# Kernel optimization log

Measured on AMD Instinct MI355X. Metric: run time of the kernel, lower is better.

## Reference

```python
import jax, jax.numpy as jnp
import numpy as np

# pywt db4 decomposition filters (8 taps)
DEC_LO = np.array([-0.010597401784997278, 0.032883011666982945, 0.030841381835986965,
                   -0.18703481171888114, -0.02798376941698385, 0.6308807679295904,
                   0.7148465705525415, 0.23037781330885523], dtype=np.float32)
DEC_HI = np.array([-0.23037781330885523, 0.7148465705525415, -0.6308807679295904,
                   -0.02798376941698385, 0.18703481171888114, 0.030841381835986965,
                   -0.032883011666982945, -0.010597401784997278], dtype=np.float32)
LEVEL = 6
F = 8  # filter length

# pywt dwt with mode='zero' is exactly full_convolve(x, filt)[1::2].
# We realize it as a strided correlation with the flipped filters:
# out[i] = sum_j x_pad[2i+j] * filt[F-1-j], x padded left by F-2 zeros.
_KERNEL = jnp.asarray(np.stack([DEC_LO[::-1], DEC_HI[::-1]])[:, None, :])  # [2,1,F]

def _dwt_step(x):
    # x: [B, N] -> (cA [B, M], cD [B, M]) with M = floor((N+F-1)/2)
    N = x.shape[-1]
    M = (N + F - 1) // 2
    xp = jnp.pad(x, ((0, 0), (F - 2, F)))[:, None, :]          # [B,1,Npad]
    y = jax.lax.conv_general_dilated(
        xp, _KERNEL.astype(x.dtype), window_strides=(2,), padding='VALID',
        dimension_numbers=('NCH', 'OIH', 'NCH'))                # [B,2,>=M]
    return y[:, 0, :M], y[:, 1, :M]


def setup_inputs() -> dict:
    key = jax.random.key(0)
    x = jax.random.normal(key, (64, 262144), dtype=jnp.float32)
    return {"x": x}


def reference(x):
    # Cascaded 6-level db4 DWT, zero boundary mode.
    a = x
    details = []  # finest first
    for _ in range(LEVEL):
        a, d = _dwt_step(a)
        details.append(d)
    # Match torch module: details[0] = coarsest detail (pywt coeffs[1])
    return (a,) + tuple(details[::-1])
```

## Files before the change

kernel.cpp:

```cpp
#include <hip/hip_runtime.h>


#define NT 256
#define TT 32
#define LEN0 2426
#define LEN1 1210
#define LEN2 602
#define LEN3 298
#define LEN4 146
#define LEN5 70

#define N0 262144
#define M1 131075
#define M2 65541
#define M3 32774
#define M4 16390
#define M5 8198
#define M6 4102

#define OFF_A6 ((size_t)0)
#define OFF_D6 ((size_t)262528)
#define OFF_D5 ((size_t)525056)
#define OFF_D4 ((size_t)1049728)
#define OFF_D3 ((size_t)2098688)
#define OFF_D2 ((size_t)4196224)
#define OFF_D1 ((size_t)8390848)

#define AE 0
#define AO 1216
#define BE 2432
#define BO 3040
#define LDS_FLOATS 3648

__device__ __constant__ float RLO[8] = {
    0.23037781330885523f, 0.7148465705525415f, 0.6308807679295904f,
    -0.02798376941698385f, -0.18703481171888114f, 0.030841381835986965f,
    0.032883011666982945f, -0.010597401784997278f};
__device__ __constant__ float RHI[8] = {
    -0.010597401784997278f, -0.032883011666982945f, 0.030841381835986965f,
    0.18703481171888114f, -0.02798376941698385f, -0.6308807679295904f,
    0.7148465705525415f, -0.23037781330885523f};

template <int LEN, int NC, int SHIFT>
__device__ __forceinline__ void level_fast(const float4* __restrict__ sE4,
                                           const float4* __restrict__ sO4,
                                           float2* __restrict__ dE2,
                                           float2* __restrict__ dO2,
                                           float* __restrict__ dg) {
  for (int c = threadIdx.x; c < NC; c += NT) {
    float4 e0 = sE4[c], e1 = sE4[c + 1];
    float4 o0 = sO4[c], o1 = sO4[c + 1];
    float e[8] = {e0.x, e0.y, e0.z, e0.w, e1.x, e1.y, e1.z, e1.w};
    float o[8] = {o0.x, o0.y, o0.z, o0.w, o1.x, o1.y, o1.z, o1.w};
    float a[4], d[4];
#pragma unroll
    for (int j = 0; j < 4; ++j) {
      float aa = 0.f, dd = 0.f;
#pragma unroll
      for (int t = 0; t < 4; ++t) {
        float ev = e[j + t + SHIFT];
        float ov = o[j + t + SHIFT];
        aa = fmaf(RLO[2 * t], ev, aa);
        aa = fmaf(RLO[2 * t + 1], ov, aa);
        dd = fmaf(RHI[2 * t], ev, dd);
        dd = fmaf(RHI[2 * t + 1], ov, dd);
      }
      a[j] = aa;
      d[j] = dd;
    }
    dE2[c] = make_float2(a[0], a[2]);
    dO2[c] = make_float2(a[1], a[3]);
    const int l0 = 4 * c;
    if (l0 + 4 <= LEN) {
#pragma unroll
      for (int j = 0; j < 4; ++j) __builtin_nontemporal_store(d[j], dg + l0 + j);
    } else {
#pragma unroll
      for (int j = 0; j < 4; ++j)
        if (l0 + j < LEN) __builtin_nontemporal_store(d[j], dg + l0 + j);
    }
  }
}

__device__ inline void dwt_step_slow(const float* __restrict__ s,
                                     float* __restrict__ d, int base, int len,
                                     int M, int cOff, float* __restrict__ dglob,
                                     int tid) {
  for (int l = tid; l < len; l += NT) {
    int g = base + l;
    float a = 0.f, dt = 0.f;
    if (g >= 0 && g < M) {
#pragma unroll
      for (int m = 0; m < 8; ++m) {
        float v = s[2 * l + m];
        a = fmaf(RLO[m], v, a);
        dt = fmaf(RHI[m], v, dt);
      }
    }
    d[l] = a;
    if (l >= cOff && g < M) dglob[g] = dt;
  }
}

__global__ __launch_bounds__(NT, 8) void dwt6_kernel(const float* __restrict__ x,
                                                     float* __restrict__ out) {
  const int p = blockIdx.x;
  const int row = blockIdx.y;
  const int tid = threadIdx.x;

  __shared__ float lds[LDS_FLOATS];

  const int b6 = p * TT;
  const int b5 = 2 * b6 - 6;
  const int b4 = 2 * b5 - 6;
  const int b3 = 2 * b4 - 6;
  const int b2 = 2 * b3 - 6;
  const int b1 = 2 * b2 - 6;
  const int b0 = 2 * b1 - 6;

  const size_t r1 = (size_t)row * M1, r2 = (size_t)row * M2,
               r3 = (size_t)row * M3, r4 = (size_t)row * M4,
               r5 = (size_t)row * M5, r6 = (size_t)row * M6;

  if (p >= 1 && p <= 127) {
    const float4* __restrict__ xs4 =
        (const float4*)(x + (size_t)row * N0 + (b0 - 2));
    float2* __restrict__ aE2 = (float2*)(lds + AE);
    float2* __restrict__ aO2 = (float2*)(lds + AO);
    for (int m = tid; m < 607; m += NT) {
      float4 v = xs4[m];
      aE2[m] = make_float2(v.x, v.z);
      aO2[m] = make_float2(v.y, v.w);
    }
    __syncthreads();

    const float4* aE4 = (const float4*)(lds + AE);
    const float4* aO4 = (const float4*)(lds + AO);
    const float4* bE4 = (const float4*)(lds + BE);
    const float4* bO4 = (const float4*)(lds + BO);
    float2* bE2 = (float2*)(lds + BE);
    float2* bO2 = (float2*)(lds + BO);

    level_fast<LEN1, 303, 1>(aE4, aO4, bE2, bO2, out + OFF_D1 + r1 + b1);
    __syncthreads();
    level_fast<LEN2, 151, 0>(bE4, bO4, aE2, aO2, out + OFF_D2 + r2 + b2);
    __syncthreads();
    level_fast<LEN3, 75, 0>(aE4, aO4, bE2, bO2, out + OFF_D3 + r3 + b3);
    __syncthreads();
    level_fast<LEN4, 37, 0>(bE4, bO4, aE2, aO2, out + OFF_D4 + r4 + b4);
    __syncthreads();
    level_fast<LEN5, 18, 0>(aE4, aO4, bE2, bO2, out + OFF_D5 + r5 + b5);
    __syncthreads();

    float* __restrict__ ga = out + OFF_A6 + r6 + b6;
    float* __restrict__ gd = out + OFF_D6 + r6 + b6;
    for (int c = tid; c < 8; c += NT) {
      float4 e0 = bE4[c], e1 = bE4[c + 1];
      float4 o0 = bO4[c], o1 = bO4[c + 1];
      float e[8] = {e0.x, e0.y, e0.z, e0.w, e1.x, e1.y, e1.z, e1.w};
      float o[8] = {o0.x, o0.y, o0.z, o0.w, o1.x, o1.y, o1.z, o1.w};
#pragma unroll
      for (int j = 0; j < 4; ++j) {
        float aa = 0.f, dd = 0.f;
#pragma unroll
        for (int t = 0; t < 4; ++t) {
          aa = fmaf(RLO[2 * t], e[j + t], aa);
          aa = fmaf(RLO[2 * t + 1], o[j + t], aa);
          dd = fmaf(RHI[2 * t], e[j + t], dd);
          dd = fmaf(RHI[2 * t + 1], o[j + t], dd);
        }
        __builtin_nontemporal_store(aa, ga + 4 * c + j);
        __builtin_nontemporal_store(dd, gd + 4 * c + j);
      }
    }
  } else {
    float* bufA = lds;
    float* bufB = lds + BE;
    const float* __restrict__ xr = x + (size_t)row * N0;
    for (int l = tid; l < LEN0; l += NT) {
      int g = b0 + l;
      bufA[l] = (g >= 0 && g < N0) ? xr[g] : 0.0f;
    }
    __syncthreads();

    dwt_step_slow(bufA, bufB, b1, LEN1, M1, 186, out + OFF_D1 + r1, tid);
    __syncthreads();
    dwt_step_slow(bufB, bufA, b2, LEN2, M2, 90, out + OFF_D2 + r2, tid);
    __syncthreads();
    dwt_step_slow(bufA, bufB, b3, LEN3, M3, 42, out + OFF_D3 + r3, tid);
    __syncthreads();
    dwt_step_slow(bufB, bufA, b4, LEN4, M4, 18, out + OFF_D4 + r4, tid);
    __syncthreads();
    dwt_step_slow(bufA, bufB, b5, LEN5, M5, 6, out + OFF_D5 + r5, tid);
    __syncthreads();

    for (int l = tid; l < TT; l += NT) {
      int g = b6 + l;
      if (g < M6) {
        float a = 0.f, dt = 0.f;
#pragma unroll
        for (int m = 0; m < 8; ++m) {
          float v = bufB[2 * l + m];
          a = fmaf(RLO[m], v, a);
          dt = fmaf(RHI[m], v, dt);
        }
        out[OFF_A6 + r6 + g] = a;
        out[OFF_D6 + r6 + g] = dt;
      }
    }
  }
}

extern "C" void kernel_launch(void* const* d_in, const int* in_sizes, int n_in,
                              void* d_out, int out_size, void* d_ws,
                              size_t ws_size, hipStream_t stream) {
  const float* x = (const float*)d_in[0];
  float* out = (float*)d_out;
  dim3 grid(129, 64);
  dwt6_kernel<<<grid, NT, 0, stream>>>(x, out);
}
```

Before: 115.8 us.

## Make blocks persistent over four tiles with register-prefetched next input

Each block now processes four consecutive tiles per row instead of one, with a separate block handling both edge tiles. While level 1 of the current tile runs, the next tile's input is loaded into registers, and it is written into the freed staging LDS after level 1 finishes. Barriers are replaced by an lgkmcnt wait plus s_barrier. This cuts the grid to a quarter of its size and overlaps global load latency with compute. In exchange there are fewer blocks to hide latency, more LDS per block, and extra register pressure from the prefetched values.

```diff
diff --git a/kernel.cpp b/kernel.cpp
--- a/kernel.cpp
+++ b/kernel.cpp
@@ -3,12 +3,7 @@
 
 #define NT 256
 #define TT 32
-#define LEN0 2426
-#define LEN1 1210
-#define LEN2 602
-#define LEN3 298
-#define LEN4 146
-#define LEN5 70
+#define ITERS 4
 
 #define N0 262144
 #define M1 131075
@@ -18,6 +13,18 @@
 #define M5 8198
 #define M6 4102
 
+#define LEN1 1210
+#define LEN2 602
+#define LEN3 298
+#define LEN4 146
+#define LEN5 70
+
+#define NC1 303
+#define NC2 151
+#define NC3 75
+#define NC4 37
+#define NC5 18
+
 #define OFF_A6 ((size_t)0)
 #define OFF_D6 ((size_t)262528)
 #define OFF_D5 ((size_t)525056)
@@ -26,11 +33,13 @@
 #define OFF_D2 ((size_t)4196224)
 #define OFF_D1 ((size_t)8390848)
 
-#define AE 0
-#define AO 1216
-#define BE 2432
-#define BO 3040
-#define LDS_FLOATS 3648
+#define SE 0
+#define SO 1216
+#define W0E 2432
+#define W0O 3040
+#define W1E 3648
+#define W1O 3952
+#define LDS_FLOATS 4256
 
 __device__ __constant__ float RLO[8] = {
     0.23037781330885523f, 0.7148465705525415f, 0.6308807679295904f,
@@ -40,6 +49,11 @@
     -0.010597401784997278f, -0.032883011666982945f, 0.030841381835986965f,
     0.18703481171888114f, -0.02798376941698385f, -0.6308807679295904f,
     0.7148465705525415f, -0.23037781330885523f};
+
+__device__ __forceinline__ void bar_lds() {
+  asm volatile("s_waitcnt lgkmcnt(0)" ::: "memory");
+  __builtin_amdgcn_s_barrier();
+}
 
 template <int LEN, int NC, int SHIFT>
 __device__ __forceinline__ void level_fast(const float4* __restrict__ sE4,
@@ -102,110 +116,173 @@
   }
 }
 
-__global__ __launch_bounds__(NT, 8) void dwt6_kernel(const float* __restrict__ x,
-                                                     float* __restrict__ out) {
-  const int p = blockIdx.x;
+__global__ __launch_bounds__(NT, 8) void dwt6_kernel(
+    const float* __restrict__ x, float* __restrict__ out) {
+  const int px = blockIdx.x;
   const int row = blockIdx.y;
   const int tid = threadIdx.x;
 
-  __shared__ float lds[LDS_FLOATS];
-
-  const int b6 = p * TT;
-  const int b5 = 2 * b6 - 6;
-  const int b4 = 2 * b5 - 6;
-  const int b3 = 2 * b4 - 6;
-  const int b2 = 2 * b3 - 6;
-  const int b1 = 2 * b2 - 6;
-  const int b0 = 2 * b1 - 6;
-
+  __shared__ __align__(16) float lds[LDS_FLOATS];
+
+  const float* __restrict__ xr = x + (size_t)row * N0;
   const size_t r1 = (size_t)row * M1, r2 = (size_t)row * M2,
                r3 = (size_t)row * M3, r4 = (size_t)row * M4,
                r5 = (size_t)row * M5, r6 = (size_t)row * M6;
 
-  if (p >= 1 && p <= 127) {
-    const float4* __restrict__ xs4 =
-        (const float4*)(x + (size_t)row * N0 + (b0 - 2));
-    float2* __restrict__ aE2 = (float2*)(lds + AE);
-    float2* __restrict__ aO2 = (float2*)(lds + AO);
-    for (int m = tid; m < 607; m += NT) {
-      float4 v = xs4[m];
-      aE2[m] = make_float2(v.x, v.z);
-      aO2[m] = make_float2(v.y, v.w);
-    }
-    __syncthreads();
-
-    const float4* aE4 = (const float4*)(lds + AE);
-    const float4* aO4 = (const float4*)(lds + AO);
-    const float4* bE4 = (const float4*)(lds + BE);
-    const float4* bO4 = (const float4*)(lds + BO);
-    float2* bE2 = (float2*)(lds + BE);
-    float2* bO2 = (float2*)(lds + BO);
-
-    level_fast<LEN1, 303, 1>(aE4, aO4, bE2, bO2, out + OFF_D1 + r1 + b1);
-    __syncthreads();
-    level_fast<LEN2, 151, 0>(bE4, bO4, aE2, aO2, out + OFF_D2 + r2 + b2);
-    __syncthreads();
-    level_fast<LEN3, 75, 0>(aE4, aO4, bE2, bO2, out + OFF_D3 + r3 + b3);
-    __syncthreads();
-    level_fast<LEN4, 37, 0>(bE4, bO4, aE2, aO2, out + OFF_D4 + r4 + b4);
-    __syncthreads();
-    level_fast<LEN5, 18, 0>(aE4, aO4, bE2, bO2, out + OFF_D5 + r5 + b5);
-    __syncthreads();
-
-    float* __restrict__ ga = out + OFF_A6 + r6 + b6;
-    float* __restrict__ gd = out + OFF_D6 + r6 + b6;
-    for (int c = tid; c < 8; c += NT) {
-      float4 e0 = bE4[c], e1 = bE4[c + 1];
-      float4 o0 = bO4[c], o1 = bO4[c + 1];
-      float e[8] = {e0.x, e0.y, e0.z, e0.w, e1.x, e1.y, e1.z, e1.w};
-      float o[8] = {o0.x, o0.y, o0.z, o0.w, o1.x, o1.y, o1.z, o1.w};
-#pragma unroll
-      for (int j = 0; j < 4; ++j) {
-        float aa = 0.f, dd = 0.f;
-#pragma unroll
-        for (int t = 0; t < 4; ++t) {
-          aa = fmaf(RLO[2 * t], e[j + t], aa);
-          aa = fmaf(RLO[2 * t + 1], o[j + t], aa);
-          dd = fmaf(RHI[2 * t], e[j + t], dd);
-          dd = fmaf(RHI[2 * t + 1], o[j + t], dd);
-        }
-        __builtin_nontemporal_store(aa, ga + 4 * c + j);
-        __builtin_nontemporal_store(dd, gd + 4 * c + j);
+  if (px < 32) {
+    float2* sE2 = (float2*)(lds + SE);
+    float2* sO2 = (float2*)(lds + SO);
+    const float4* sE4 = (const float4*)(lds + SE);
+    const float4* sO4 = (const float4*)(lds + SO);
+    float2* w0E2 = (float2*)(lds + W0E);
+    float2* w0O2 = (float2*)(lds + W0O);
+    float2* w1E2 = (float2*)(lds + W1E);
+    float2* w1O2 = (float2*)(lds + W1O);
+    const float4* w0E4 = (const float4*)(lds + W0E);
+    const float4* w0O4 = (const float4*)(lds + W0O);
+    const float4* w1E4 = (const float4*)(lds + W1E);
+    const float4* w1O4 = (const float4*)(lds + W1O);
+
+    const int p0 = 1 + ITERS * px;
+
+    {
+      const float4* __restrict__ xs4 = (const float4*)(xr + (2048 * p0 - 380));
+      float4 v0 = xs4[tid];
+      float4 v1, v2;
+      if (tid < 351) v1 = xs4[tid + 256];
+      if (tid < 95) v2 = xs4[tid + 512];
+      sE2[tid] = make_float2(v0.x, v0.z);
+      sO2[tid] = make_float2(v0.y, v0.w);
+      if (tid < 351) {
+        sE2[tid + 256] = make_float2(v1.x, v1.z);
+        sO2[tid + 256] = make_float2(v1.y, v1.w);
+      }
+      if (tid < 95) {
+        sE2[tid + 512] = make_float2(v2.x, v2.z);
+        sO2[tid + 512] = make_float2(v2.y, v2.w);
+      }
+    }
+
+#pragma unroll 1
+    for (int k = 0; k < ITERS; ++k) {
+      const int p = p0 + k;
+      if (p > 127) break;
+      const bool have_next = (k + 1 < ITERS) && (p + 1 <= 127);
+
+      float4 q0, q1, q2;
+      if (have_next) {
+        const float4* __restrict__ xn4 =
+            (const float4*)(xr + (2048 * (p + 1) - 380));
+        q0 = xn4[tid];
+        if (tid < 351) q1 = xn4[tid + 256];
+        if (tid < 95) q2 = xn4[tid + 512];
+      }
+
+      const int b6 = p * TT;
+      const int b5 = 2 * b6 - 6;
+      const int b4 = 2 * b5 - 6;
+      const int b3 = 2 * b4 - 6;
+      const int b2 = 2 * b3 - 6;
+      const int b1 = 2 * b2 - 6;
+
+      bar_lds();
+
+      level_fast<LEN1, NC1, 1>(sE4, sO4, w0E2, w0O2, out + OFF_D1 + r1 + b1);
+      bar_lds();
+
+      if (have_next) {
+        sE2[tid] = make_float2(q0.x, q0.z);
+        sO2[tid] = make_float2(q0.y, q0.w);
+        if (tid < 351) {
+          sE2[tid + 256] = make_float2(q1.x, q1.z);
+          sO2[tid + 256] = make_float2(q1.y, q1.w);
+        }
+        if (tid < 95) {
+          sE2[tid + 512] = make_float2(q2.x, q2.z);
+          sO2[tid + 512] = make_float2(q2.y, q2.w);
+        }
+      }
+
+      level_fast<LEN2, NC2, 0>(w0E4, w0O4, w1E2, w1O2,
+                               out + OFF_D2 + r2 + b2);
+      bar_lds();
+      level_fast<LEN3, NC3, 0>(w1E4, w1O4, w0E2, w0O2,
+                               out + OFF_D3 + r3 + b3);
+      bar_lds();
+      level_fast<LEN4, NC4, 0>(w0E4, w0O4, w1E2, w1O2,
+                               out + OFF_D4 + r4 + b4);
+      bar_lds();
+      level_fast<LEN5, NC5, 0>(w1E4, w1O4, w0E2, w0O2,
+                               out + OFF_D5 + r5 + b5);
+      bar_lds();
+
+      float* __restrict__ ga = out + OFF_A6 + r6 + b6;
+      float* __restrict__ gd = out + OFF_D6 + r6 + b6;
+      for (int c = tid; c < 8; c += NT) {
+        float4 e0 = w0E4[c], e1 = w0E4[c + 1];
+        float4 o0 = w0O4[c], o1 = w0O4[c + 1];
+        float e[8] = {e0.x, e0.y, e0.z, e0.w, e1.x, e1.y, e1.z, e1.w};
+        float o[8] = {o0.x, o0.y, o0.z, o0.w, o1.x, o1.y, o1.z, o1.w};
+#pragma unroll
+        for (int j = 0; j < 4; ++j) {
+          float aa = 0.f, dd = 0.f;
+#pragma unroll
+          for (int t = 0; t < 4; ++t) {
+            aa = fmaf(RLO[2 * t], e[j + t], aa);
+            aa = fmaf(RLO[2 * t + 1], o[j + t], aa);
+            dd = fmaf(RHI[2 * t], e[j + t], dd);
+            dd = fmaf(RHI[2 * t + 1], o[j + t], dd);
+          }
+          __builtin_nontemporal_store(aa, ga + 4 * c + j);
+          __builtin_nontemporal_store(dd, gd + 4 * c + j);
+        }
       }
     }
   } else {
-    float* bufA = lds;
-    float* bufB = lds + BE;
-    const float* __restrict__ xr = x + (size_t)row * N0;
-    for (int l = tid; l < LEN0; l += NT) {
-      int g = b0 + l;
-      bufA[l] = (g >= 0 && g < N0) ? xr[g] : 0.0f;
-    }
-    __syncthreads();
-
-    dwt_step_slow(bufA, bufB, b1, LEN1, M1, 186, out + OFF_D1 + r1, tid);
-    __syncthreads();
-    dwt_step_slow(bufB, bufA, b2, LEN2, M2, 90, out + OFF_D2 + r2, tid);
-    __syncthreads();
-    dwt_step_slow(bufA, bufB, b3, LEN3, M3, 42, out + OFF_D3 + r3, tid);
-    __syncthreads();
-    dwt_step_slow(bufB, bufA, b4, LEN4, M4, 18, out + OFF_D4 + r4, tid);
-    __syncthreads();
-    dwt_step_slow(bufA, bufB, b5, LEN5, M5, 6, out + OFF_D5 + r5, tid);
-    __syncthreads();
-
-    for (int l = tid; l < TT; l += NT) {
-      int g = b6 + l;
-      if (g < M6) {
-        float a = 0.f, dt = 0.f;
-#pragma unroll
-        for (int m = 0; m < 8; ++m) {
-          float v = bufB[2 * l + m];
-          a = fmaf(RLO[m], v, a);
-          dt = fmaf(RHI[m], v, dt);
-        }
-        out[OFF_A6 + r6 + g] = a;
-        out[OFF_D6 + r6 + g] = dt;
+    float* A = lds;
+    float* B = lds + W0E;
+#pragma unroll 1
+    for (int t = 0; t < 2; ++t) {
+      const int p = (t == 0) ? 0 : 128;
+      const int b6 = p * TT;
+      const int b5 = 2 * b6 - 6;
+      const int b4 = 2 * b5 - 6;
+      const int b3 = 2 * b4 - 6;
+      const int b2 = 2 * b3 - 6;
+      const int b1 = 2 * b2 - 6;
+      const int b0 = 2 * b1 - 6;
+
+      bar_lds();
+      for (int l = tid; l < 2426; l += NT) {
+        int g = b0 + l;
+        A[l] = (g >= 0 && g < N0) ? xr[g] : 0.0f;
+      }
+      bar_lds();
+
+      dwt_step_slow(A, B, b1, LEN1, M1, 186, out + OFF_D1 + r1, tid);
+      bar_lds();
+      dwt_step_slow(B, A, b2, LEN2, M2, 90, out + OFF_D2 + r2, tid);
+      bar_lds();
+      dwt_step_slow(A, B, b3, LEN3, M3, 42, out + OFF_D3 + r3, tid);
+      bar_lds();
+      dwt_step_slow(B, A, b4, LEN4, M4, 18, out + OFF_D4 + r4, tid);
+      bar_lds();
+      dwt_step_slow(A, B, b5, LEN5, M5, 6, out + OFF_D5 + r5, tid);
+      bar_lds();
+
+      for (int l = tid; l < TT; l += NT) {
+        int g = b6 + l;
+        if (g < M6) {
+          float a = 0.f, dt = 0.f;
+#pragma unroll
+          for (int m = 0; m < 8; ++m) {
+            float v = B[2 * l + m];
+            a = fmaf(RLO[m], v, a);
+            dt = fmaf(RHI[m], v, dt);
+          }
+          out[OFF_A6 + r6 + g] = a;
+          out[OFF_D6 + r6 + g] = dt;
+        }
       }
     }
   }
@@ -216,6 +293,6 @@
                               size_t ws_size, hipStream_t stream) {
   const float* x = (const float*)d_in[0];
   float* out = (float*)d_out;
-  dim3 grid(129, 64);
+  dim3 grid(33, 64);
   dwt6_kernel<<<grid, NT, 0, stream>>>(x, out);
 }
```

After: 124.6 us. 7.6% more time.

## Give each wavefront its own DWT tile and drop block-wide barriers

Applied to the files above, without the earlier changes.

Tiles are halved and each of the four wavefronts in a block now runs its own independent 6-level cascade in a private LDS slice. Block-wide __syncthreads are replaced by a wave-local lgkmcnt wait. The first level is computed directly from global float4 loads, removing the LDS staging pass. The boundary tiles (p=0, 255, 256) are handled in a loop by one extra block per row, and the grid shrinks accordingly. The cost is more halo recomputation per output from the smaller tiles, and correctness depends on the wave-local LDS fence being enough for intra-wave LDS reuse.

```diff
diff --git a/kernel.cpp b/kernel.cpp
--- a/kernel.cpp
+++ b/kernel.cpp
@@ -2,13 +2,7 @@
 
 
 #define NT 256
-#define TT 32
-#define LEN0 2426
-#define LEN1 1210
-#define LEN2 602
-#define LEN3 298
-#define LEN4 146
-#define LEN5 70
+#define TT 16
 
 #define N0 262144
 #define M1 131075
@@ -18,6 +12,19 @@
 #define M5 8198
 #define M6 4102
 
+#define NC1 190
+#define NC2 94
+#define NC3 46
+#define NC4 22
+#define NC5 10
+
+#define LEN0S 1402
+#define LEN1S 698
+#define LEN2S 346
+#define LEN3S 170
+#define LEN4S 82
+#define LEN5S 38
+
 #define OFF_A6 ((size_t)0)
 #define OFF_D6 ((size_t)262528)
 #define OFF_D5 ((size_t)525056)
@@ -26,11 +33,12 @@
 #define OFF_D2 ((size_t)4196224)
 #define OFF_D1 ((size_t)8390848)
 
-#define AE 0
-#define AO 1216
-#define BE 2432
-#define BO 3040
-#define LDS_FLOATS 3648
+#define W0E 0
+#define W0O 384
+#define W1E 768
+#define W1O 960
+#define WSLICE 1152
+#define LDS_FLOATS (4 * WSLICE)
 
 __device__ __constant__ float RLO[8] = {
     0.23037781330885523f, 0.7148465705525415f, 0.6308807679295904f,
@@ -41,44 +49,48 @@
     0.18703481171888114f, -0.02798376941698385f, -0.6308807679295904f,
     0.7148465705525415f, -0.23037781330885523f};
 
-template <int LEN, int NC, int SHIFT>
-__device__ __forceinline__ void level_fast(const float4* __restrict__ sE4,
-                                           const float4* __restrict__ sO4,
-                                           float2* __restrict__ dE2,
-                                           float2* __restrict__ dO2,
-                                           float* __restrict__ dg) {
-  for (int c = threadIdx.x; c < NC; c += NT) {
+__device__ __forceinline__ void fence_lds() {
+  asm volatile("s_waitcnt lgkmcnt(0)" ::: "memory");
+}
+
+template <int SHIFT>
+__device__ __forceinline__ void conv8(const float e[8], const float o[8],
+                                      float a[4], float d[4]) {
+#pragma unroll
+  for (int j = 0; j < 4; ++j) {
+    float aa = 0.f, dd = 0.f;
+#pragma unroll
+    for (int t = 0; t < 4; ++t) {
+      float ev = e[j + t + SHIFT];
+      float ov = o[j + t + SHIFT];
+      aa = fmaf(RLO[2 * t], ev, aa);
+      aa = fmaf(RLO[2 * t + 1], ov, aa);
+      dd = fmaf(RHI[2 * t], ev, dd);
+      dd = fmaf(RHI[2 * t + 1], ov, dd);
+    }
+    a[j] = aa;
+    d[j] = dd;
+  }
+}
+
+template <int NC>
+__device__ __forceinline__ void level_w(const float4* __restrict__ sE4,
+                                        const float4* __restrict__ sO4,
+                                        float2* __restrict__ dE2,
+                                        float2* __restrict__ dO2,
+                                        float* __restrict__ dg, int lane) {
+  for (int c = lane; c < NC; c += 64) {
     float4 e0 = sE4[c], e1 = sE4[c + 1];
     float4 o0 = sO4[c], o1 = sO4[c + 1];
     float e[8] = {e0.x, e0.y, e0.z, e0.w, e1.x, e1.y, e1.z, e1.w};
     float o[8] = {o0.x, o0.y, o0.z, o0.w, o1.x, o1.y, o1.z, o1.w};
     float a[4], d[4];
-#pragma unroll
-    for (int j = 0; j < 4; ++j) {
-      float aa = 0.f, dd = 0.f;
-#pragma unroll
-      for (int t = 0; t < 4; ++t) {
-        float ev = e[j + t + SHIFT];
-        float ov = o[j + t + SHIFT];
-        aa = fmaf(RLO[2 * t], ev, aa);
-        aa = fmaf(RLO[2 * t + 1], ov, aa);
-        dd = fmaf(RHI[2 * t], ev, dd);
-        dd = fmaf(RHI[2 * t + 1], ov, dd);
-      }
-      a[j] = aa;
-      d[j] = dd;
-    }
+    conv8<0>(e, o, a, d);
     dE2[c] = make_float2(a[0], a[2]);
     dO2[c] = make_float2(a[1], a[3]);
     const int l0 = 4 * c;
-    if (l0 + 4 <= LEN) {
-#pragma unroll
-      for (int j = 0; j < 4; ++j) __builtin_nontemporal_store(d[j], dg + l0 + j);
-    } else {
-#pragma unroll
-      for (int j = 0; j < 4; ++j)
-        if (l0 + j < LEN) __builtin_nontemporal_store(d[j], dg + l0 + j);
-    }
+#pragma unroll
+    for (int j = 0; j < 4; ++j) __builtin_nontemporal_store(d[j], dg + l0 + j);
   }
 }
 
@@ -102,110 +114,138 @@
   }
 }
 
-__global__ __launch_bounds__(NT, 8) void dwt6_kernel(const float* __restrict__ x,
-                                                     float* __restrict__ out) {
-  const int p = blockIdx.x;
+__global__ __launch_bounds__(NT, 8) void dwt6_kernel(
+    const float* __restrict__ x, float* __restrict__ out) {
+  const int px = blockIdx.x;
   const int row = blockIdx.y;
   const int tid = threadIdx.x;
 
-  __shared__ float lds[LDS_FLOATS];
-
-  const int b6 = p * TT;
-  const int b5 = 2 * b6 - 6;
-  const int b4 = 2 * b5 - 6;
-  const int b3 = 2 * b4 - 6;
-  const int b2 = 2 * b3 - 6;
-  const int b1 = 2 * b2 - 6;
-  const int b0 = 2 * b1 - 6;
-
+  __shared__ __align__(16) float lds[LDS_FLOATS];
+
+  const float* __restrict__ xr = x + (size_t)row * N0;
   const size_t r1 = (size_t)row * M1, r2 = (size_t)row * M2,
                r3 = (size_t)row * M3, r4 = (size_t)row * M4,
                r5 = (size_t)row * M5, r6 = (size_t)row * M6;
 
-  if (p >= 1 && p <= 127) {
-    const float4* __restrict__ xs4 =
-        (const float4*)(x + (size_t)row * N0 + (b0 - 2));
-    float2* __restrict__ aE2 = (float2*)(lds + AE);
-    float2* __restrict__ aO2 = (float2*)(lds + AO);
-    for (int m = tid; m < 607; m += NT) {
-      float4 v = xs4[m];
-      aE2[m] = make_float2(v.x, v.z);
-      aO2[m] = make_float2(v.y, v.w);
-    }
-    __syncthreads();
-
-    const float4* aE4 = (const float4*)(lds + AE);
-    const float4* aO4 = (const float4*)(lds + AO);
-    const float4* bE4 = (const float4*)(lds + BE);
-    const float4* bO4 = (const float4*)(lds + BO);
-    float2* bE2 = (float2*)(lds + BE);
-    float2* bO2 = (float2*)(lds + BO);
-
-    level_fast<LEN1, 303, 1>(aE4, aO4, bE2, bO2, out + OFF_D1 + r1 + b1);
-    __syncthreads();
-    level_fast<LEN2, 151, 0>(bE4, bO4, aE2, aO2, out + OFF_D2 + r2 + b2);
-    __syncthreads();
-    level_fast<LEN3, 75, 0>(aE4, aO4, bE2, bO2, out + OFF_D3 + r3 + b3);
-    __syncthreads();
-    level_fast<LEN4, 37, 0>(bE4, bO4, aE2, aO2, out + OFF_D4 + r4 + b4);
-    __syncthreads();
-    level_fast<LEN5, 18, 0>(aE4, aO4, bE2, bO2, out + OFF_D5 + r5 + b5);
-    __syncthreads();
-
-    float* __restrict__ ga = out + OFF_A6 + r6 + b6;
-    float* __restrict__ gd = out + OFF_D6 + r6 + b6;
-    for (int c = tid; c < 8; c += NT) {
-      float4 e0 = bE4[c], e1 = bE4[c + 1];
-      float4 o0 = bO4[c], o1 = bO4[c + 1];
+  if (px < 64) {
+    const int wv = tid >> 6;
+    const int lane = tid & 63;
+    const int p = 1 + 4 * px + wv;
+    if (p > 254) return;
+
+    float* __restrict__ W = lds + wv * WSLICE;
+    float2* w0E2 = (float2*)(W + W0E);
+    float2* w0O2 = (float2*)(W + W0O);
+    float2* w1E2 = (float2*)(W + W1E);
+    float2* w1O2 = (float2*)(W + W1O);
+    const float4* w0E4 = (const float4*)(W + W0E);
+    const float4* w0O4 = (const float4*)(W + W0O);
+    const float4* w1E4 = (const float4*)(W + W1E);
+    const float4* w1O4 = (const float4*)(W + W1O);
+
+    const int b6 = 16 * p;
+    const int b5 = 32 * p - 6;
+    const int b4 = 64 * p - 18;
+    const int b3 = 128 * p - 42;
+    const int b2 = 256 * p - 90;
+    const int b1 = 512 * p - 186;
+
+    {
+      const float4* __restrict__ x4 = (const float4*)(xr + (1024 * p - 380));
+      float* __restrict__ dg1 = out + OFF_D1 + r1 + b1;
+      for (int c = lane; c < NC1; c += 64) {
+        float4 q0 = x4[2 * c], q1 = x4[2 * c + 1];
+        float4 q2 = x4[2 * c + 2], q3 = x4[2 * c + 3];
+        float e[8] = {q0.x, q0.z, q1.x, q1.z, q2.x, q2.z, q3.x, q3.z};
+        float o[8] = {q0.y, q0.w, q1.y, q1.w, q2.y, q2.w, q3.y, q3.w};
+        float a[4], d[4];
+        conv8<1>(e, o, a, d);
+        w0E2[c] = make_float2(a[0], a[2]);
+        w0O2[c] = make_float2(a[1], a[3]);
+        const int l0 = 4 * c;
+#pragma unroll
+        for (int j = 0; j < 4; ++j)
+          __builtin_nontemporal_store(d[j], dg1 + l0 + j);
+      }
+    }
+    fence_lds();
+
+    level_w<NC2>(w0E4, w0O4, w1E2, w1O2, out + OFF_D2 + r2 + b2, lane);
+    fence_lds();
+    level_w<NC3>(w1E4, w1O4, w0E2, w0O2, out + OFF_D3 + r3 + b3, lane);
+    fence_lds();
+    level_w<NC4>(w0E4, w0O4, w1E2, w1O2, out + OFF_D4 + r4 + b4, lane);
+    fence_lds();
+    level_w<NC5>(w1E4, w1O4, w0E2, w0O2, out + OFF_D5 + r5 + b5, lane);
+    fence_lds();
+
+    if (lane < 4) {
+      const int c = lane;
+      float* __restrict__ ga = out + OFF_A6 + r6 + b6;
+      float* __restrict__ gd = out + OFF_D6 + r6 + b6;
+      float4 e0 = w0E4[c], e1 = w0E4[c + 1];
+      float4 o0 = w0O4[c], o1 = w0O4[c + 1];
       float e[8] = {e0.x, e0.y, e0.z, e0.w, e1.x, e1.y, e1.z, e1.w};
       float o[8] = {o0.x, o0.y, o0.z, o0.w, o1.x, o1.y, o1.z, o1.w};
+      float a[4], d[4];
+      conv8<0>(e, o, a, d);
+      const int l0 = 4 * c;
 #pragma unroll
       for (int j = 0; j < 4; ++j) {
-        float aa = 0.f, dd = 0.f;
-#pragma unroll
-        for (int t = 0; t < 4; ++t) {
-          aa = fmaf(RLO[2 * t], e[j + t], aa);
-          aa = fmaf(RLO[2 * t + 1], o[j + t], aa);
-          dd = fmaf(RHI[2 * t], e[j + t], dd);
-          dd = fmaf(RHI[2 * t + 1], o[j + t], dd);
+        __builtin_nontemporal_store(a[j], ga + l0 + j);
+        __builtin_nontemporal_store(d[j], gd + l0 + j);
+      }
+    }
+  } else {
+    float* A = lds;
+    float* B = lds + 1408;
+#pragma unroll 1
+    for (int t = 0; t < 3; ++t) {
+      const int p = (t == 0) ? 0 : (t == 1) ? 255 : 256;
+      const int b6 = 16 * p;
+      const int b5 = 32 * p - 6;
+      const int b4 = 64 * p - 18;
+      const int b3 = 128 * p - 42;
+      const int b2 = 256 * p - 90;
+      const int b1 = 512 * p - 186;
+      const int b0 = 1024 * p - 378;
+      const int c1 = (p == 0) ? 186 : 0;
+      const int c2 = (p == 0) ? 90 : 0;
+      const int c3 = (p == 0) ? 42 : 0;
+      const int c4 = (p == 0) ? 18 : 0;
+      const int c5 = (p == 0) ? 6 : 0;
+
+      __syncthreads();
+      for (int l = tid; l < LEN0S; l += NT) {
+        int g = b0 + l;
+        A[l] = (g >= 0 && g < N0) ? xr[g] : 0.0f;
+      }
+      __syncthreads();
+
+      dwt_step_slow(A, B, b1, LEN1S, M1, c1, out + OFF_D1 + r1, tid);
+      __syncthreads();
+      dwt_step_slow(B, A, b2, LEN2S, M2, c2, out + OFF_D2 + r2, tid);
+      __syncthreads();
+      dwt_step_slow(A, B, b3, LEN3S, M3, c3, out + OFF_D3 + r3, tid);
+      __syncthreads();
+      dwt_step_slow(B, A, b4, LEN4S, M4, c4, out + OFF_D4 + r4, tid);
+      __syncthreads();
+      dwt_step_slow(A, B, b5, LEN5S, M5, c5, out + OFF_D5 + r5, tid);
+      __syncthreads();
+
+      for (int l = tid; l < TT; l += NT) {
+        int g = b6 + l;
+        if (g < M6) {
+          float a = 0.f, dt = 0.f;
+#pragma unroll
+          for (int m = 0; m < 8; ++m) {
+            float v = B[2 * l + m];
+            a = fmaf(RLO[m], v, a);
+            dt = fmaf(RHI[m], v, dt);
+          }
+          out[OFF_A6 + r6 + g] = a;
+          out[OFF_D6 + r6 + g] = dt;
         }
-        __builtin_nontemporal_store(aa, ga + 4 * c + j);
-        __builtin_nontemporal_store(dd, gd + 4 * c + j);
-      }
-    }
-  } else {
-    float* bufA = lds;
-    float* bufB = lds + BE;
-    const float* __restrict__ xr = x + (size_t)row * N0;
-    for (int l = tid; l < LEN0; l += NT) {
-      int g = b0 + l;
-      bufA[l] = (g >= 0 && g < N0) ? xr[g] : 0.0f;
-    }
-    __syncthreads();
-
-    dwt_step_slow(bufA, bufB, b1, LEN1, M1, 186, out + OFF_D1 + r1, tid);
-    __syncthreads();
-    dwt_step_slow(bufB, bufA, b2, LEN2, M2, 90, out + OFF_D2 + r2, tid);
-    __syncthreads();
-    dwt_step_slow(bufA, bufB, b3, LEN3, M3, 42, out + OFF_D3 + r3, tid);
-    __syncthreads();
-    dwt_step_slow(bufB, bufA, b4, LEN4, M4, 18, out + OFF_D4 + r4, tid);
-    __syncthreads();
-    dwt_step_slow(bufA, bufB, b5, LEN5, M5, 6, out + OFF_D5 + r5, tid);
-    __syncthreads();
-
-    for (int l = tid; l < TT; l += NT) {
-      int g = b6 + l;
-      if (g < M6) {
-        float a = 0.f, dt = 0.f;
-#pragma unroll
-        for (int m = 0; m < 8; ++m) {
-          float v = bufB[2 * l + m];
-          a = fmaf(RLO[m], v, a);
-          dt = fmaf(RHI[m], v, dt);
-        }
-        out[OFF_A6 + r6 + g] = a;
-        out[OFF_D6 + r6 + g] = dt;
       }
     }
   }
@@ -216,6 +256,6 @@
                               size_t ws_size, hipStream_t stream) {
   const float* x = (const float*)d_in[0];
   float* out = (float*)d_out;
-  dim3 grid(129, 64);
+  dim3 grid(65, 64);
   dwt6_kernel<<<grid, NT, 0, stream>>>(x, out);
 }
```

Measured after the change: 117.4 us. About the same (+1.4%).
